# Kernel tuning notes

Hardware: AMD Instinct MI355X
Metric: run time of the kernel (lower is better)

## Reference

```python
import jax, jax.numpy as jnp
import numpy as np
import math

B, S, D, H = 2, 2048, 2048, 16
HD = D // H  # 128


def _rope(x, cos, sin):
    # x: [b, s, h, hd]; cos/sin: [s, hd//2]
    # torch view_as_complex pairs adjacent elements: (even=real, odd=imag)
    xr = x[..., 0::2]
    xi = x[..., 1::2]
    c = cos[None, :, None, :]
    s = sin[None, :, None, :]
    out_r = xr * c - xi * s
    out_i = xr * s + xi * c
    # interleave back: [..., hd//2, 2] -> [..., hd]
    return jnp.stack([out_r, out_i], axis=-1).reshape(x.shape)


def setup_inputs() -> dict:
    key = jax.random.key(0)
    ks = jax.random.split(key, 5)
    x = jax.random.normal(ks[0], (B, S, D), dtype=jnp.float32)
    std = 1.0 / math.sqrt(D)
    wq = jax.random.normal(ks[1], (D, D), dtype=jnp.float32) * std
    wk = jax.random.normal(ks[2], (D, D), dtype=jnp.float32) * std
    wv = jax.random.normal(ks[3], (D, D), dtype=jnp.float32) * std
    wo = jax.random.normal(ks[4], (D, D), dtype=jnp.float32) * std
    # RoPE frequencies, theta = 10000
    freqs = 1.0 / (10000.0 ** (jnp.arange(0, HD, 2, dtype=jnp.float32) / HD))  # [hd//2]
    t = jnp.arange(S, dtype=jnp.float32)
    angles = jnp.outer(t, freqs)  # [s, hd//2]
    freqs_cos = jnp.cos(angles)
    freqs_sin = jnp.sin(angles)
    # causal additive mask [s, s]
    mask = jnp.triu(jnp.full((S, S), -jnp.inf, dtype=jnp.float32), k=1)
    return {"x": x, "start_pos": 0, "freqs_cos": freqs_cos, "freqs_sin": freqs_sin,
            "mask": mask, "wq": wq, "wk": wk, "wv": wv, "wo": wo}


def reference(x, start_pos, freqs_cos, freqs_sin, mask, wq, wk, wv, wo):
    b, s, d = x.shape
    # projections (torch Linear: y = x @ W.T)
    xq = (x @ wq.T).reshape(b, s, H, HD)
    xk = (x @ wk.T).reshape(b, s, H, HD)
    xv = (x @ wv.T).reshape(b, s, H, HD)
    xq = _rope(xq, freqs_cos, freqs_sin)
    xk = _rope(xk, freqs_cos, freqs_sin)
    # start_pos = 0 prefill: cache[:b, :s] == freshly computed xk/xv
    # scores: [b, h, s_q, s_k]
    scores = jnp.einsum("bqhd,bkhd->bhqk", xq, xk) / math.sqrt(HD)
    scores = scores + mask[None, None, :, :]
    probs = jax.nn.softmax(scores, axis=-1)
    out = jnp.einsum("bhqk,bkhd->bqhd", probs, xv).reshape(b, s, d)
    return out @ wo.T
```

## Files before the change

kernel.cpp:

```cpp
#include <hip/hip_runtime.h>

typedef __attribute__((ext_vector_type(8))) short short8;
typedef __attribute__((ext_vector_type(4))) float f32x4;
typedef __attribute__((ext_vector_type(16))) float f32x16;
typedef unsigned int u32;
typedef __attribute__((ext_vector_type(4))) u32 u32x4;
typedef unsigned short u16;

#define DEV __device__ __forceinline__

DEV void async16(const void* g, void* l) {
  __builtin_amdgcn_global_load_lds((const __attribute__((address_space(1))) u32*)g,
                                   (__attribute__((address_space(3))) u32*)l, 16, 0, 0);
}

DEV u16 f2bf(float f) {
  u32 u = __builtin_bit_cast(u32, f);
  u32 r = (u + 0x7FFFu + ((u >> 16) & 1u)) >> 16;
  return (u16)r;
}
DEV float bf2f(u16 h) { return __builtin_bit_cast(float, (u32)h << 16); }

DEV u32 cvtpk(float lo, float hi) {
  u32 r;
  asm("v_cvt_pk_bf16_f32 %0, %1, %2" : "=v"(r) : "v"(lo), "v"(hi));
  return r;
}

__global__ void cast_all_kernel(const float* __restrict__ x, const float* __restrict__ wq,
                                const float* __restrict__ wk, const float* __restrict__ wv,
                                const float* __restrict__ wo, u16* __restrict__ out) {
  constexpr int XN = 2097152;
  constexpr int WN = 1048576;
  constexpr int TOT = XN + 4 * WN;
  int stride = gridDim.x * blockDim.x;
  for (int i = blockIdx.x * blockDim.x + threadIdx.x; i < TOT; i += stride) {
    const float* src;
    int off;
    if (i < XN) {
      src = x; off = i;
    } else {
      int j = i - XN, wsel = j >> 20;
      const float* ws4[4] = {wq, wk, wv, wo};
      src = ws4[wsel]; off = j & (WN - 1);
    }
    float4 v = reinterpret_cast<const float4*>(src)[off];
    ushort4 o = make_ushort4(f2bf(v.x), f2bf(v.y), f2bf(v.z), f2bf(v.w));
    reinterpret_cast<ushort4*>(out)[i] = o;
  }
}

template <int MODE>
__global__ __launch_bounds__(256) void gemm_bt(const u16* __restrict__ A,
                                               const u16* __restrict__ Bw,
                                               void* __restrict__ C0,
                                               u16* __restrict__ C1,
                                               u16* __restrict__ C2) {
  constexpr int K = 2048;
  __shared__ char sm[32768];
  const int tid = threadIdx.x;
  const int lane = tid & 63;
  const int w = tid >> 6;
  const int by = blockIdx.x & 31;
  const int bx = blockIdx.x >> 5;
  const int row0 = by * 128, col0 = bx * 128;
  const int wr = (w >> 1) * 64, wc = (w & 1) * 64;
  f32x4 acc[4][4] = {};

  for (int k0 = 0; k0 < K; k0 += 64) {
    __syncthreads();
#pragma unroll
    for (int i = 0; i < 4; ++i) {
      int slot = tid + i * 256;
      int r = slot >> 3, s = slot & 7;
      int sl = s ^ (r & 7);
      async16(A + (size_t)(row0 + r) * K + (k0 + sl * 8), sm + slot * 16);
    }
#pragma unroll
    for (int i = 0; i < 4; ++i) {
      int slot = tid + i * 256;
      int r = slot >> 3, s = slot & 7;
      int sl = s ^ (r & 7);
      async16(Bw + (size_t)(col0 + r) * K + (k0 + sl * 8), sm + 16384 + slot * 16);
    }
    __syncthreads();
#pragma unroll
    for (int kk = 0; kk < 2; ++kk) {
      short8 af[4], bfr[4];
#pragma unroll
      for (int mi = 0; mi < 4; ++mi) {
        int r = wr + mi * 16 + (lane & 15);
        int ps = (kk * 4 + (lane >> 4)) ^ (r & 7);
        af[mi] = *reinterpret_cast<const short8*>(sm + r * 128 + ps * 16);
      }
#pragma unroll
      for (int ni = 0; ni < 4; ++ni) {
        int r = wc + ni * 16 + (lane & 15);
        int ps = (kk * 4 + (lane >> 4)) ^ (r & 7);
        bfr[ni] = *reinterpret_cast<const short8*>(sm + 16384 + r * 128 + ps * 16);
      }
#pragma unroll
      for (int mi = 0; mi < 4; ++mi)
#pragma unroll
        for (int ni = 0; ni < 4; ++ni)
          acc[mi][ni] = __builtin_amdgcn_mfma_f32_16x16x32_bf16(af[mi], bfr[ni], acc[mi][ni], 0, 0, 0);
    }
  }
#pragma unroll
  for (int mi = 0; mi < 4; ++mi)
#pragma unroll
    for (int ni = 0; ni < 4; ++ni)
#pragma unroll
      for (int r = 0; r < 4; ++r) {
        int gm = row0 + wr + mi * 16 + ((lane >> 4) << 2) + r;
        int gn = col0 + wc + ni * 16 + (lane & 15);
        float v = acc[mi][ni][r];
        if constexpr (MODE == 4) {
          int tsel = gn >> 11, nn = gn & 2047;
          int b = gm >> 11, s = gm & 2047, h = nn >> 7, hd = nn & 127;
          u16* dst = (tsel == 0) ? (u16*)C0 : (tsel == 1) ? C1 : C2;
          if (tsel < 2)
            dst[(size_t)((b << 4) | h) * 262144 + (s << 7) + hd] = f2bf(v);
          else
            dst[(size_t)((b << 4) | h) * 262144 + (hd << 11) + s] = f2bf(v);
        } else {
          ((float*)C0)[((size_t)gm << 11) + gn] = v;
        }
      }
}

__global__ void rope_kernel(u16* __restrict__ q, u16* __restrict__ k,
                            const float* __restrict__ cb, const float* __restrict__ sb) {
  const float rs = 0.127517436f;
  const int NP = 2 * 16 * 2048 * 64;
  int stride = gridDim.x * blockDim.x;
  for (int i = blockIdx.x * blockDim.x + threadIdx.x; i < 2 * NP; i += stride) {
    int p = (i < NP) ? i : i - NP;
    u16* base = (i < NP) ? q : k;
    float sc = (i < NP) ? rs : 1.0f;
    int fi = p & 63;
    int s = (p >> 6) & 2047;
    u32 v = *reinterpret_cast<u32*>(base + 2 * (size_t)p);
    float xr = bf2f((u16)(v & 0xFFFFu)), xi = bf2f((u16)(v >> 16));
    float c = cb[(s << 6) + fi], sn = sb[(s << 6) + fi];
    float orr = (xr * c - xi * sn) * sc;
    float oi = (xr * sn + xi * c) * sc;
    *reinterpret_cast<u32*>(base + 2 * (size_t)p) = (u32)f2bf(orr) | ((u32)f2bf(oi) << 16);
  }
}

__global__ __launch_bounds__(256, 2) void attn_kernel(const u16* __restrict__ q_ws,
                                                      const u16* __restrict__ k_ws,
                                                      const u16* __restrict__ vt_ws,
                                                      u16* __restrict__ attn_ws) {
  constexpr int S = 2048;
  constexpr float NEGBIG = -3.0e38f;
  __shared__ char sm[65536];
  const int tid = threadIdx.x, lane = tid & 63, w = tid >> 6;
  const int hi = lane >> 5, l31 = lane & 31;
  const int bid = blockIdx.x;
  const int qtr = bid >> 5;
  const int qt = (qtr < 8) ? qtr : 23 - qtr;
  const int bh = ((bid & 7) << 2) | ((bid >> 3) & 3);
  const int qr0 = qt * 128 + w * 32;
  const int ntile = 2 * qt + 2;
  const int my_nt = (qr0 >> 6) + 1;

  const u16* qp = q_ws + (size_t)bh * S * 128;
  const u16* kp = k_ws + (size_t)bh * S * 128;
  const u16* vp = vt_ws + (size_t)bh * 128 * S;

  short8 qf[8];
  {
    const u16* qr = qp + (size_t)(qr0 + l31) * 128 + hi * 8;
#pragma unroll
    for (int ks = 0; ks < 8; ++ks) qf[ks] = *reinterpret_cast<const short8*>(qr + ks * 16);
  }
  f32x16 accO[4];
#pragma unroll
  for (int dc = 0; dc < 4; ++dc)
#pragma unroll
    for (int r = 0; r < 16; ++r) accO[dc][r] = 0.f;
  float m = -1e30f, l = 0.f;

  auto stage = [&](int bufoff, int kv0) {
#pragma unroll
    for (int i = 0; i < 4; ++i) {
      int slot = tid + i * 256;
      int r = slot >> 4, s = slot & 15;
      async16(kp + (size_t)(kv0 + r) * 128 + ((s ^ (r & 15)) * 8), sm + bufoff + slot * 16);
    }
#pragma unroll
    for (int i = 0; i < 4; ++i) {
      int slot = tid + i * 256;
      int r = slot >> 3, s = slot & 7;
      async16(vp + (size_t)r * S + kv0 + ((s ^ (r & 7)) * 8), sm + bufoff + 16384 + slot * 16);
    }
  };

  stage(0, 0);
  __syncthreads();

  for (int t = 0; t < ntile; ++t) {
    const char* kb = sm + (t & 1) * 32768;
    const char* vb = kb + 16384;
    if (t + 1 < ntile) stage(((t + 1) & 1) * 32768, (t + 1) * 64);

    if (t < my_nt) {
      f32x16 sacc[2];
#pragma unroll
      for (int jc = 0; jc < 2; ++jc)
#pragma unroll
        for (int r = 0; r < 16; ++r) sacc[jc][r] = 0.f;
      __builtin_amdgcn_s_setprio(1);
#pragma unroll
      for (int jc = 0; jc < 2; ++jc) {
        const char* krp = kb + (jc * 32 + l31) * 256;
        const int sw = l31 & 15;
#pragma unroll
        for (int ks = 0; ks < 8; ++ks) {
          short8 kf = *reinterpret_cast<const short8*>(krp + (((2 * ks + hi) ^ sw) << 4));
          sacc[jc] = __builtin_amdgcn_mfma_f32_32x32x16_bf16(kf, qf[ks], sacc[jc], 0, 0, 0);
        }
      }
      __builtin_amdgcn_s_setprio(0);
      if (t == my_nt - 1) {
#pragma unroll
        for (int jc = 0; jc < 2; ++jc) {
          int thr = qr0 + l31 - t * 64 - 32 * jc - 4 * hi;
#pragma unroll
          for (int r = 0; r < 16; ++r) {
            int c0 = (r & 3) + 8 * (r >> 2);
            if (c0 > thr) sacc[jc][r] = NEGBIG;
          }
        }
      }
      float pmA = NEGBIG, pmB = NEGBIG, pmC = NEGBIG, pmD = NEGBIG;
#pragma unroll
      for (int jc = 0; jc < 2; ++jc)
#pragma unroll
        for (int r = 0; r < 16; r += 4) {
          pmA = fmaxf(pmA, sacc[jc][r]);
          pmB = fmaxf(pmB, sacc[jc][r + 1]);
          pmC = fmaxf(pmC, sacc[jc][r + 2]);
          pmD = fmaxf(pmD, sacc[jc][r + 3]);
        }
      float pmax = fmaxf(fmaxf(pmA, pmB), fmaxf(pmC, pmD));
      pmax = fmaxf(pmax, __shfl_xor(pmax, 32, 64));
      if (!__all(pmax - m <= 8.0f)) {
        float mnew = fmaxf(m, pmax);
        float scl = exp2f(m - mnew);
        m = mnew;
        l *= scl;
#pragma unroll
        for (int dc = 0; dc < 4; ++dc)
#pragma unroll
          for (int r = 0; r < 16; ++r) accO[dc][r] *= scl;
      }
      float sA = 0.f, sB = 0.f, sC = 0.f, sD = 0.f;
#pragma unroll
      for (int jc = 0; jc < 2; ++jc)
#pragma unroll
        for (int r = 0; r < 16; r += 4) {
          float p0 = exp2f(sacc[jc][r] - m);
          float p1 = exp2f(sacc[jc][r + 1] - m);
          float p2 = exp2f(sacc[jc][r + 2] - m);
          float p3 = exp2f(sacc[jc][r + 3] - m);
          sacc[jc][r] = p0; sacc[jc][r + 1] = p1; sacc[jc][r + 2] = p2; sacc[jc][r + 3] = p3;
          sA += p0; sB += p1; sC += p2; sD += p3;
        }
      float ps = (sA + sB) + (sC + sD);
      ps += __shfl_xor(ps, 32, 64);
      l += ps;
      short8 pfrag[4];
#pragma unroll
      for (int ks = 0; ks < 4; ++ks) {
        const int jc = ks >> 1, u8 = (ks & 1) * 8;
        u32 wA = cvtpk(sacc[jc][u8 + 0], sacc[jc][u8 + 1]);
        u32 wB = cvtpk(sacc[jc][u8 + 2], sacc[jc][u8 + 3]);
        u32 wC = cvtpk(sacc[jc][u8 + 4], sacc[jc][u8 + 5]);
        u32 wD = cvtpk(sacc[jc][u8 + 6], sacc[jc][u8 + 7]);
        u32 qA = __shfl_xor(wA, 32, 64);
        u32 qB = __shfl_xor(wB, 32, 64);
        u32 qC = __shfl_xor(wC, 32, 64);
        u32 qD = __shfl_xor(wD, 32, 64);
        u32x4 t4;
        t4.x = hi ? qC : wA;
        t4.y = hi ? qD : wB;
        t4.z = hi ? wC : qA;
        t4.w = hi ? wD : qB;
        pfrag[ks] = __builtin_bit_cast(short8, t4);
      }
      __builtin_amdgcn_s_setprio(1);
#pragma unroll
      for (int ks = 0; ks < 4; ++ks) {
#pragma unroll
        for (int dc = 0; dc < 4; ++dc) {
          const char* vrp = vb + (dc * 32 + l31) * 128;
          short8 vf = *reinterpret_cast<const short8*>(vrp + (((2 * ks + hi) ^ (l31 & 7)) << 4));
          accO[dc] = __builtin_amdgcn_mfma_f32_32x32x16_bf16(vf, pfrag[ks], accO[dc], 0, 0, 0);
        }
      }
      __builtin_amdgcn_s_setprio(0);
    }
    __syncthreads();
  }

  const int b = bh >> 4, h = bh & 15;
  char* tb = sm + w * 8192;
  float inv = (l > 0.f) ? 1.0f / l : 0.f;
#pragma unroll
  for (int dc = 0; dc < 4; ++dc)
#pragma unroll
    for (int r = 0; r < 16; ++r) {
      int d = dc * 32 + (r & 3) + 8 * (r >> 2) + 4 * hi;
      int byte = l31 * 256 + d * 2;
      *reinterpret_cast<u16*>(tb + (byte ^ ((l31 & 7) << 4))) = f2bf(accO[dc][r] * inv);
    }
  asm volatile("s_waitcnt lgkmcnt(0)" ::: "memory");
#pragma unroll
  for (int i = 0; i < 8; ++i) {
    int r = i * 4 + (lane >> 4);
    int s = lane & 15;
    f32x4 v = *reinterpret_cast<const f32x4*>(tb + r * 256 + ((s ^ (r & 7)) << 4));
    size_t addr = ((size_t)(b * 2048 + qr0 + r) << 11) + (h << 7) + s * 8;
    *reinterpret_cast<f32x4*>(attn_ws + addr) = v;
  }
}

extern "C" void kernel_launch(void* const* d_in, const int* in_sizes, int n_in,
                              void* d_out, int out_size, void* d_ws, size_t ws_size,
                              hipStream_t stream) {
  const float* x = (const float*)d_in[0];
  const float* cb = (const float*)d_in[2];
  const float* sb = (const float*)d_in[3];
  const float* wq = (const float*)d_in[5];
  const float* wk = (const float*)d_in[6];
  const float* wv = (const float*)d_in[7];
  const float* wo = (const float*)d_in[8];

  char* p = (char*)d_ws;
  u16* xb  = (u16*)p; p += (size_t)4096 * 2048 * 2;
  u16* wqb = (u16*)p; p += (size_t)2048 * 2048 * 2;
  u16* wkb = (u16*)p; p += (size_t)2048 * 2048 * 2;
  u16* wvb = (u16*)p; p += (size_t)2048 * 2048 * 2;
  u16* wob = (u16*)p; p += (size_t)2048 * 2048 * 2;
  u16* q_ws = (u16*)p; p += (size_t)4096 * 2048 * 2;
  u16* k_ws = (u16*)p; p += (size_t)4096 * 2048 * 2;
  u16* vt_ws = (u16*)p; p += (size_t)4096 * 2048 * 2;
  u16* attn_ws = xb;
  (void)wkb; (void)wvb;

  cast_all_kernel<<<3072, 256, 0, stream>>>(x, wq, wk, wv, wo, xb);

  gemm_bt<4><<<1536, 256, 0, stream>>>(xb, wqb, q_ws, k_ws, vt_ws);

  rope_kernel<<<2048, 256, 0, stream>>>(q_ws, k_ws, cb, sb);

  attn_kernel<<<512, 256, 0, stream>>>(q_ws, k_ws, vt_ws, attn_ws);

  gemm_bt<3><<<512, 256, 0, stream>>>(attn_ws, wob, d_out, nullptr, nullptr);
}
```

Before: 271.8 us.

## Replace QKV GEMM with 256x256 pipelined 8-wave kernel and fuse RoPE epilogue

Adds a new QKV projection kernel with 256x256 tiles, 8 waves, and 128 KB LDS double-buffered async staging. Global loads are interleaved with MFMA phases using raw barriers, vmcnt waits and setprio. RoPE and the query scale are applied in the epilogue through a lane shuffle, which removes the separate rope kernel and its extra read-write pass over Q and K. The design depends on the manual waitcnt and barrier schedule being correct, and 128 KB of LDS per block limits occupancy.

```diff
diff --git a/kernel.cpp b/kernel.cpp
--- a/kernel.cpp
+++ b/kernel.cpp
@@ -26,6 +26,9 @@
   asm("v_cvt_pk_bf16_f32 %0, %1, %2" : "=v"(r) : "v"(lo), "v"(hi));
   return r;
 }
+
+#define RAW_BARRIER() asm volatile("s_barrier" ::: "memory")
+#define VMWAIT(N) asm volatile("s_waitcnt vmcnt(" #N ")" ::: "memory")
 
 __global__ void cast_all_kernel(const float* __restrict__ x, const float* __restrict__ wq,
                                 const float* __restrict__ wk, const float* __restrict__ wv,
@@ -50,12 +53,156 @@
   }
 }
 
-template <int MODE>
+__global__ __launch_bounds__(512, 2) void gemm_qkv8(const u16* __restrict__ A,
+                                                    const u16* __restrict__ Bw,
+                                                    u16* __restrict__ q_ws,
+                                                    u16* __restrict__ k_ws,
+                                                    u16* __restrict__ vt_ws,
+                                                    const float* __restrict__ cbp,
+                                                    const float* __restrict__ sbp) {
+  constexpr int K = 2048, NT = 32;
+  __shared__ char sm[131072];
+  const int tid = threadIdx.x, lane = tid & 63, w = tid >> 6;
+  const int wm = w >> 2, wn = w & 3;
+  const int bid = blockIdx.x;
+  const int n = (bid & 7) * 48 + (bid >> 3);
+  const int row0 = (n & 15) * 256, col0 = (n >> 4) * 256;
+
+  f32x4 acc[2][2][4][2] = {};
+
+  auto stage_chunk = [&](int bufoff, int chunk, int k0) {
+    const bool isA = (chunk == 0) || (chunk == 3);
+    const u16* src = isA ? A : Bw;
+    const int h = isA ? ((chunk == 3) ? 1 : 0) : (chunk - 1);
+    const int rbase = (isA ? row0 : col0) + h * 128;
+    const int ldsbase = bufoff + (isA ? 0 : 32768) + h * 16384;
+#pragma unroll
+    for (int i = 0; i < 2; ++i) {
+      int slot = tid + i * 512;
+      int r = slot >> 3, cs = slot & 7;
+      async16(src + (size_t)(rbase + r) * K + k0 + ((cs ^ (r & 7)) << 3),
+              sm + ldsbase + slot * 16);
+    }
+  };
+
+  short8 af[4][2], bf0[2][2], bf1[2][2];
+  auto ldA = [&](int base, int ha) {
+#pragma unroll
+    for (int mi = 0; mi < 4; ++mi) {
+      int row = ha * 128 + wm * 64 + mi * 16 + (lane & 15);
+#pragma unroll
+      for (int kk = 0; kk < 2; ++kk)
+        af[mi][kk] = *reinterpret_cast<const short8*>(
+            sm + base + row * 128 + ((((kk << 2) + (lane >> 4)) ^ (row & 7)) << 4));
+    }
+  };
+  auto ldB = [&](short8 (&bf)[2][2], int base, int hb) {
+#pragma unroll
+    for (int ni = 0; ni < 2; ++ni) {
+      int row = hb * 128 + wn * 32 + ni * 16 + (lane & 15);
+#pragma unroll
+      for (int kk = 0; kk < 2; ++kk)
+        bf[ni][kk] = *reinterpret_cast<const short8*>(
+            sm + base + 32768 + row * 128 + ((((kk << 2) + (lane >> 4)) ^ (row & 7)) << 4));
+    }
+  };
+
+#define MFMA16(HA, HB, BF)                                                              \
+  __builtin_amdgcn_s_setprio(1);                                                        \
+  _Pragma("unroll") for (int mi = 0; mi < 4; ++mi)                                      \
+      _Pragma("unroll") for (int ni = 0; ni < 2; ++ni)                                  \
+          _Pragma("unroll") for (int kk = 0; kk < 2; ++kk)                              \
+              acc[HA][HB][mi][ni] = __builtin_amdgcn_mfma_f32_16x16x32_bf16(            \
+                  af[mi][kk], BF[ni][kk], acc[HA][HB][mi][ni], 0, 0, 0);                \
+  __builtin_amdgcn_s_setprio(0);
+
+  stage_chunk(0, 0, 0);
+  stage_chunk(0, 1, 0);
+  stage_chunk(0, 2, 0);
+  stage_chunk(0, 3, 0);
+  VMWAIT(0);
+  RAW_BARRIER();
+
+  for (int t = 0; t < NT - 1; ++t) {
+    const int cb_ = (t & 1) * 65536, nb = ((t + 1) & 1) * 65536;
+    const int k0n = (t + 1) * 64;
+    ldA(cb_, 0);
+    ldB(bf0, cb_, 0);
+    stage_chunk(nb, 0, k0n);
+    RAW_BARRIER();
+    MFMA16(0, 0, bf0);
+    VMWAIT(4);
+    RAW_BARRIER();
+    ldB(bf1, cb_, 1);
+    stage_chunk(nb, 1, k0n);
+    RAW_BARRIER();
+    MFMA16(0, 1, bf1);
+    VMWAIT(4);
+    RAW_BARRIER();
+    ldA(cb_, 1);
+    stage_chunk(nb, 2, k0n);
+    RAW_BARRIER();
+    MFMA16(1, 0, bf0);
+    RAW_BARRIER();
+    stage_chunk(nb, 3, k0n);
+    RAW_BARRIER();
+    MFMA16(1, 1, bf1);
+    VMWAIT(4);
+    RAW_BARRIER();
+  }
+  {
+    const int cb_ = ((NT - 1) & 1) * 65536;
+    ldA(cb_, 0);
+    ldB(bf0, cb_, 0);
+    RAW_BARRIER();
+    MFMA16(0, 0, bf0);
+    VMWAIT(0);
+    RAW_BARRIER();
+    ldB(bf1, cb_, 1);
+    RAW_BARRIER();
+    MFMA16(0, 1, bf1);
+    RAW_BARRIER();
+    ldA(cb_, 1);
+    RAW_BARRIER();
+    MFMA16(1, 0, bf0);
+    RAW_BARRIER();
+    MFMA16(1, 1, bf1);
+  }
+
+  const float rs = 0.127517436f;
+#pragma unroll
+  for (int ha = 0; ha < 2; ++ha)
+#pragma unroll
+    for (int hb = 0; hb < 2; ++hb)
+#pragma unroll
+      for (int mi = 0; mi < 4; ++mi)
+#pragma unroll
+        for (int ni = 0; ni < 2; ++ni)
+#pragma unroll
+          for (int rr = 0; rr < 4; ++rr) {
+            int gm = row0 + ha * 128 + wm * 64 + mi * 16 + ((lane >> 4) << 2) + rr;
+            int gn = col0 + hb * 128 + wn * 32 + ni * 16 + (lane & 15);
+            float v = acc[ha][hb][mi][ni][rr];
+            int tsel = gn >> 11, nn = gn & 2047;
+            int b = gm >> 11, s = gm & 2047, h = nn >> 7, hd = nn & 127;
+            if (tsel < 2) {
+              float pv = __shfl_xor(v, 1, 64);
+              float c = cbp[(s << 6) + (hd >> 1)];
+              float sn = sbp[(s << 6) + (hd >> 1)];
+              float o = (hd & 1) ? (pv * sn + v * c) : (v * c - pv * sn);
+              if (tsel == 0) o *= rs;
+              u16* dst = tsel ? k_ws : q_ws;
+              dst[(size_t)((b << 4) | h) * 262144 + (s << 7) + hd] = f2bf(o);
+            } else {
+              vt_ws[(size_t)((b << 4) | h) * 262144 + (hd << 11) + s] = f2bf(v);
+            }
+          }
+#undef MFMA16
+}
+
 __global__ __launch_bounds__(256) void gemm_bt(const u16* __restrict__ A,
                                                const u16* __restrict__ Bw,
-                                               void* __restrict__ C0,
-                                               u16* __restrict__ C1,
-                                               u16* __restrict__ C2) {
+                                               float* __restrict__ C) {
   constexpr int K = 2048;
   __shared__ char sm[32768];
   const int tid = threadIdx.x;
@@ -114,39 +261,8 @@
       for (int r = 0; r < 4; ++r) {
         int gm = row0 + wr + mi * 16 + ((lane >> 4) << 2) + r;
         int gn = col0 + wc + ni * 16 + (lane & 15);
-        float v = acc[mi][ni][r];
-        if constexpr (MODE == 4) {
-          int tsel = gn >> 11, nn = gn & 2047;
-          int b = gm >> 11, s = gm & 2047, h = nn >> 7, hd = nn & 127;
-          u16* dst = (tsel == 0) ? (u16*)C0 : (tsel == 1) ? C1 : C2;
-          if (tsel < 2)
-            dst[(size_t)((b << 4) | h) * 262144 + (s << 7) + hd] = f2bf(v);
-          else
-            dst[(size_t)((b << 4) | h) * 262144 + (hd << 11) + s] = f2bf(v);
-        } else {
-          ((float*)C0)[((size_t)gm << 11) + gn] = v;
-        }
-      }
-}
-
-__global__ void rope_kernel(u16* __restrict__ q, u16* __restrict__ k,
-                            const float* __restrict__ cb, const float* __restrict__ sb) {
-  const float rs = 0.127517436f;
-  const int NP = 2 * 16 * 2048 * 64;
-  int stride = gridDim.x * blockDim.x;
-  for (int i = blockIdx.x * blockDim.x + threadIdx.x; i < 2 * NP; i += stride) {
-    int p = (i < NP) ? i : i - NP;
-    u16* base = (i < NP) ? q : k;
-    float sc = (i < NP) ? rs : 1.0f;
-    int fi = p & 63;
-    int s = (p >> 6) & 2047;
-    u32 v = *reinterpret_cast<u32*>(base + 2 * (size_t)p);
-    float xr = bf2f((u16)(v & 0xFFFFu)), xi = bf2f((u16)(v >> 16));
-    float c = cb[(s << 6) + fi], sn = sb[(s << 6) + fi];
-    float orr = (xr * c - xi * sn) * sc;
-    float oi = (xr * sn + xi * c) * sc;
-    *reinterpret_cast<u32*>(base + 2 * (size_t)p) = (u32)f2bf(orr) | ((u32)f2bf(oi) << 16);
-  }
+        C[((size_t)gm << 11) + gn] = acc[mi][ni][r];
+      }
 }
 
 __global__ __launch_bounds__(256, 2) void attn_kernel(const u16* __restrict__ q_ws,
@@ -353,11 +469,9 @@
 
   cast_all_kernel<<<3072, 256, 0, stream>>>(x, wq, wk, wv, wo, xb);
 
-  gemm_bt<4><<<1536, 256, 0, stream>>>(xb, wqb, q_ws, k_ws, vt_ws);
-
-  rope_kernel<<<2048, 256, 0, stream>>>(q_ws, k_ws, cb, sb);
+  gemm_qkv8<<<384, 512, 0, stream>>>(xb, wqb, q_ws, k_ws, vt_ws, cb, sb);
 
   attn_kernel<<<512, 256, 0, stream>>>(q_ws, k_ws, vt_ws, attn_ws);
 
-  gemm_bt<3><<<512, 256, 0, stream>>>(attn_ws, wob, d_out, nullptr, nullptr);
-}
+  gemm_bt<<<512, 256, 0, stream>>>(attn_ws, wob, (float*)d_out);
+}
```

Result: slower. 296.7 us (+9.2%).
